# Kernel tuning notes

Measured on AMD Instinct MI355X. Metric: run time of the kernel, lower is better.

Reference implementation:

```python
import jax, jax.numpy as jnp
import numpy as np

EP = 1e-4
MAX_ITER = 100
NEG = -1e9
H = 8


def _layernorm(x, g, b, eps=1e-5):
    m = jnp.mean(x, axis=-1, keepdims=True)
    v = jnp.mean((x - m) ** 2, axis=-1, keepdims=True)
    return (x - m) * jax.lax.rsqrt(v + eps) * g + b


def _nonsat(x):
    # Fixed-point iteration y_{n+1} = (2 y^3/3 + x)/(y^2 + 1); torch detaches y each
    # step, so gradient only flows through x in the final update.
    xs = jax.lax.stop_gradient(x)

    def step(y):
        y2 = y * y
        return (2.0 * y * y2 / 3.0 + xs) / (y2 + 1.0)

    def cond(st):
        y, yn, i = st
        return jnp.logical_and(jnp.mean(jnp.abs(yn - y)) > EP, i <= MAX_ITER)

    def body(st):
        y, yn, i = st
        return (yn, step(yn), i + 1)

    y_prev, _, _ = jax.lax.while_loop(cond, body, (xs, step(xs), jnp.int32(0)))
    y2 = y_prev * y_prev
    return (2.0 * y_prev * y2 / 3.0 + x) / (y2 + 1.0)


def setup_inputs() -> dict:
    key = jax.random.key(0)
    ks = jax.random.split(key, 20)
    S, B, E = 256, 64, 512
    DH, SW, DSS, DFF, DEPTH = 512, 64, 128, 2048, 32
    sd = 0.02
    inp = {
        'x_in': jax.random.normal(ks[0], (S, B, E), jnp.float32),
        'stack_prev': jax.random.normal(ks[1], (B, S, DEPTH, SW), jnp.float32),
        'k_mask': jnp.zeros((B, S), jnp.bool_),
        'ln1_g': jnp.ones((E,), jnp.float32),
        'ln1_b': jnp.zeros((E,), jnp.float32),
        'in_proj_w': jax.random.normal(ks[2], (E, 3 * E), jnp.float32) * sd,
        'in_proj_b': jnp.zeros((3 * E,), jnp.float32),
        'out_w': jax.random.normal(ks[3], (E, E), jnp.float32) * sd,
        'out_b': jnp.zeros((E,), jnp.float32),
        'W_w': jax.random.normal(ks[4], (E, DH), jnp.float32) * sd,
        'W_b': jnp.zeros((DH,), jnp.float32),
        'P_w': jax.random.normal(ks[5], (SW, DH), jnp.float32) * sd,
        'P_b': jnp.zeros((DH,), jnp.float32),
        'V_w': jax.random.normal(ks[6], (E + DH, DSS), jnp.float32) * sd,
        'U_w': jax.random.normal(ks[7], (DSS, E), jnp.float32) * sd,
        'A_w': jax.random.normal(ks[8], (DH, 3), jnp.float32) * sd,
        'A_b': jnp.zeros((3,), jnp.float32),
        'D_w': jax.random.normal(ks[9], (DH, SW), jnp.float32) * sd,
        'D_b': jnp.zeros((SW,), jnp.float32),
        'ln2_g': jnp.ones((E,), jnp.float32),
        'ln2_b': jnp.zeros((E,), jnp.float32),
        'ff1_w': jax.random.normal(ks[10], (E, DFF), jnp.float32) * sd,
        'ff1_b': jnp.zeros((DFF,), jnp.float32),
        'ff2_w': jax.random.normal(ks[11], (DFF, E), jnp.float32) * sd,
        'ff2_b': jnp.zeros((E,), jnp.float32),
    }
    return inp


def reference(x_in, stack_prev, k_mask, ln1_g, ln1_b, in_proj_w, in_proj_b, out_w,
              out_b, W_w, W_b, P_w, P_b, V_w, U_w, A_w, A_b, D_w, D_b, ln2_g,
              ln2_b, ff1_w, ff1_b, ff2_w, ff2_b):
    S, B, E = x_in.shape
    hd = E // H
    scale = 1.0 / np.sqrt(hd)

    # --- sublayer 0: pre-norm causal self-attention ---
    xn = _layernorm(x_in, ln1_g, ln1_b)
    qkv = xn @ in_proj_w + in_proj_b            # (S,B,3E)
    q, k, v = jnp.split(qkv, 3, axis=-1)
    q = q.reshape(S, B, H, hd)
    k = k.reshape(S, B, H, hd)
    v = v.reshape(S, B, H, hd)
    scores = jnp.einsum('sbhd,tbhd->bhst', q, k) * scale
    causal = jnp.triu(jnp.full((S, S), NEG, x_in.dtype), k=1)
    scores = scores + causal
    scores = jnp.where(k_mask[:, None, None, :], NEG, scores)
    attn = jax.nn.softmax(scores, axis=-1)
    ao = jnp.einsum('bhst,tbhd->sbhd', attn, v).reshape(S, B, E)
    x = x_in + ao @ out_w + out_b

    # --- stack-augmented memory ---
    stack_x = stack_prev[:, :, 0, :]            # (B,S,SW) top of stack
    xb = jnp.transpose(x, (1, 0, 2))            # (B,S,E)
    hidden = _nonsat(xb @ W_w + W_b + stack_x @ P_w + P_b)  # (B,S,DH)
    vx = jnp.concatenate([x, jnp.transpose(hidden, (1, 0, 2))], axis=-1)
    y = jax.nn.softmax(vx @ V_w, axis=-1) @ U_w
    x = jnp.maximum(x, y)

    stack_inp = _nonsat(hidden @ D_w + D_b)[:, :, None, :]   # (B,S,1,SW)
    ctrl = jax.nn.softmax(hidden @ A_w + A_b, axis=-1)[..., None, None]  # (B,S,3,1,1)
    zeros = jnp.zeros_like(stack_prev[:, :, :1])
    stack_down = jnp.concatenate([stack_prev[:, :, 1:], zeros], axis=2)
    stack_up = jnp.concatenate([stack_inp, stack_prev[:, :, :-1]], axis=2)
    stack = ctrl[:, :, 2] * stack_prev + ctrl[:, :, 0] * stack_up + ctrl[:, :, 1] * stack_down

    # --- sublayer 1: pre-norm FFN ---
    xn2 = _layernorm(x, ln2_g, ln2_b)
    x = x + jax.nn.relu(xn2 @ ff1_w + ff1_b) @ ff2_w + ff2_b
    return (x, stack)
```

## Files before the change

kernel.cpp:

```cpp
#include <hip/hip_runtime.h>
#include <math.h>

#define S_DIM 256
#define B_DIM 64
#define E_DIM 512
#define H_NUM 8
#define HD 64
#define DH 512
#define SW 64
#define DSS 128
#define DFF 2048
#define DEPTH 32
#define M_ROWS 16384

typedef __attribute__((ext_vector_type(8))) short bf16x8;
typedef __attribute__((ext_vector_type(4))) float f32x4;

__device__ __forceinline__ ushort f2bf(float v){
    unsigned int u = __float_as_uint(v);
    u += 0x7fffu + ((u >> 16) & 1u);
    return (ushort)(u >> 16);
}
__device__ __forceinline__ float bf2f(ushort s){
    return __uint_as_float(((unsigned int)s) << 16);
}
__device__ __forceinline__ void splitbf(float v, ushort& h, ushort& l){
    h = f2bf(v);
    l = f2bf(v - bf2f(h));
}

__device__ __forceinline__ float nonsat_f(float x){
    float y = x;
#pragma unroll
    for (int i = 0; i < 10; i++){
        float y2 = y * y;
        y = (0.66666666f * y * y2 + x) / (y2 + 1.0f);
    }
    return y;
}

__global__ __launch_bounds__(256) void ln_split(const float* __restrict__ x,
                                                const float* __restrict__ g,
                                                const float* __restrict__ bta,
                                                ushort* __restrict__ oh,
                                                ushort* __restrict__ ol){
    __shared__ float red[4];
    int r = blockIdx.x;
    int t = threadIdx.x;
    const float* xr = x + (size_t)r * E_DIM;
    float v0 = xr[t], v1 = xr[t + 256];
    float s = v0 + v1;
#pragma unroll
    for (int off = 32; off > 0; off >>= 1) s += __shfl_xor(s, off, 64);
    if ((t & 63) == 0) red[t >> 6] = s;
    __syncthreads();
    float mean = (red[0] + red[1] + red[2] + red[3]) * (1.0f / 512.0f);
    __syncthreads();
    float d0 = v0 - mean, d1 = v1 - mean;
    float q = d0 * d0 + d1 * d1;
#pragma unroll
    for (int off = 32; off > 0; off >>= 1) q += __shfl_xor(q, off, 64);
    if ((t & 63) == 0) red[t >> 6] = q;
    __syncthreads();
    float var = (red[0] + red[1] + red[2] + red[3]) * (1.0f / 512.0f);
    float rs = rsqrtf(var + 1e-5f);
    size_t base = (size_t)r * E_DIM;
    float y0 = d0 * rs * g[t]       + bta[t];
    float y1 = d1 * rs * g[t + 256] + bta[t + 256];
    ushort h, l;
    splitbf(y0, h, l); oh[base + t] = h;       ol[base + t] = l;
    splitbf(y1, h, l); oh[base + t + 256] = h; ol[base + t + 256] = l;
}

__global__ __launch_bounds__(256) void wsplit_t(const float* __restrict__ W,
                                                ushort* __restrict__ th,
                                                ushort* __restrict__ tl,
                                                int K, int N){
    __shared__ float tile[32][33];
    int n0 = blockIdx.x << 5, k0 = blockIdx.y << 5;
    int tx = threadIdx.x & 31, ty = threadIdx.x >> 5;
#pragma unroll
    for (int i = 0; i < 32; i += 8)
        tile[ty + i][tx] = W[(size_t)(k0 + ty + i) * N + (n0 + tx)];
    __syncthreads();
#pragma unroll
    for (int i = 0; i < 32; i += 8){
        int n = ty + i;
        float v = tile[tx][n];
        ushort h, l; splitbf(v, h, l);
        th[(size_t)(n0 + n) * K + (k0 + tx)] = h;
        tl[(size_t)(n0 + n) * K + (k0 + tx)] = l;
    }
}

__global__ __launch_bounds__(256) void gemm_bf3(
    const ushort* __restrict__ Ah, const ushort* __restrict__ Al,
    const ushort* __restrict__ Bh, const ushort* __restrict__ Bl,
    const float* __restrict__ bias, const float* __restrict__ res,
    float* __restrict__ Cf, ushort* __restrict__ Ch, ushort* __restrict__ Cl,
    int M, int N, int K, int act, int resmode)
{
    __shared__ ushort lds[16384];
    const int tid = threadIdx.x;
    const int n0 = blockIdx.x << 7, m0 = blockIdx.y << 7;

    const int srow = tid >> 2, schunk = tid & 3;
    const int sOff = srow * 32 + (((srow + schunk) & 3) << 3);
    const ushort* gA0 = Ah + (size_t)(m0 + srow) * K + (schunk << 3);
    const ushort* gA1 = Al + (size_t)(m0 + srow) * K + (schunk << 3);
    const ushort* gB0 = Bh + (size_t)(n0 + srow) * K + (schunk << 3);
    const ushort* gB1 = Bl + (size_t)(n0 + srow) * K + (schunk << 3);
    const size_t rstep = (size_t)64 * K;

    const int lane = tid & 63;
    const int wv = tid >> 6;
    const int wm = (wv >> 1) << 6, wn = (wv & 1) << 6;
    const int r0 = lane & 15, gq = lane >> 4;
    const int gsub = (gq & 1) << 2;
    const int gc = gq >> 1;

    f32x4 acc[4][4];
    f32x4 zero = {0.f, 0.f, 0.f, 0.f};
#pragma unroll
    for (int i = 0; i < 4; i++)
#pragma unroll
        for (int j = 0; j < 4; j++) acc[i][j] = zero;

    uint4 v0,v1,v2,v3,v4,v5,v6,v7;
    v0 = *(const uint4*)(gA0);          v1 = *(const uint4*)(gA0 + rstep);
    v2 = *(const uint4*)(gA1);          v3 = *(const uint4*)(gA1 + rstep);
    v4 = *(const uint4*)(gB0);          v5 = *(const uint4*)(gB0 + rstep);
    v6 = *(const uint4*)(gB1);          v7 = *(const uint4*)(gB1 + rstep);

    for (int k0 = 0; k0 < K; k0 += 32){
        __syncthreads();
        *(uint4*)(&lds[sOff])               = v0;
        *(uint4*)(&lds[sOff + 2048])        = v1;
        *(uint4*)(&lds[4096 + sOff])        = v2;
        *(uint4*)(&lds[4096 + sOff + 2048]) = v3;
        *(uint4*)(&lds[8192 + sOff])        = v4;
        *(uint4*)(&lds[8192 + sOff + 2048]) = v5;
        *(uint4*)(&lds[12288 + sOff])        = v6;
        *(uint4*)(&lds[12288 + sOff + 2048]) = v7;
        __syncthreads();
        if (k0 + 32 < K){
            gA0 += 32; gA1 += 32; gB0 += 32; gB1 += 32;
            v0 = *(const uint4*)(gA0);  v1 = *(const uint4*)(gA0 + rstep);
            v2 = *(const uint4*)(gA1);  v3 = *(const uint4*)(gA1 + rstep);
            v4 = *(const uint4*)(gB0);  v5 = *(const uint4*)(gB0 + rstep);
            v6 = *(const uint4*)(gB1);  v7 = *(const uint4*)(gB1 + rstep);
        }
        bf16x8 fa[4], fal[4];
#pragma unroll
        for (int fr = 0; fr < 4; fr++){
            int R = wm + (fr << 4) + r0;
            int base = R * 32 + gsub;
            int c0 = ((gc + R) & 3) << 3;
            int c1 = ((gc + 2 + R) & 3) << 3;
            uint2 p0 = *(const uint2*)(&lds[base + c0]);
            uint2 p1 = *(const uint2*)(&lds[base + c1]);
            union { unsigned int u[4]; bf16x8 v; } t0;
            t0.u[0] = p0.x; t0.u[1] = p0.y; t0.u[2] = p1.x; t0.u[3] = p1.y;
            fa[fr] = t0.v;
            uint2 q0 = *(const uint2*)(&lds[4096 + base + c0]);
            uint2 q1 = *(const uint2*)(&lds[4096 + base + c1]);
            union { unsigned int u[4]; bf16x8 v; } t1;
            t1.u[0] = q0.x; t1.u[1] = q0.y; t1.u[2] = q1.x; t1.u[3] = q1.y;
            fal[fr] = t1.v;
        }
#pragma unroll
        for (int fc = 0; fc < 4; fc++){
            int R = wn + (fc << 4) + r0;
            int base = R * 32 + gsub;
            int c0 = ((gc + R) & 3) << 3;
            int c1 = ((gc + 2 + R) & 3) << 3;
            uint2 p0 = *(const uint2*)(&lds[8192 + base + c0]);
            uint2 p1 = *(const uint2*)(&lds[8192 + base + c1]);
            union { unsigned int u[4]; bf16x8 v; } t0;
            t0.u[0] = p0.x; t0.u[1] = p0.y; t0.u[2] = p1.x; t0.u[3] = p1.y;
            bf16x8 fbh = t0.v;
            uint2 q0 = *(const uint2*)(&lds[12288 + base + c0]);
            uint2 q1 = *(const uint2*)(&lds[12288 + base + c1]);
            union { unsigned int u[4]; bf16x8 v; } t1;
            t1.u[0] = q0.x; t1.u[1] = q0.y; t1.u[2] = q1.x; t1.u[3] = q1.y;
            bf16x8 fbl = t1.v;
#pragma unroll
            for (int fr = 0; fr < 4; fr++){
                acc[fr][fc] = __builtin_amdgcn_mfma_f32_16x16x32_bf16(fa[fr],  fbh, acc[fr][fc], 0, 0, 0);
                acc[fr][fc] = __builtin_amdgcn_mfma_f32_16x16x32_bf16(fa[fr],  fbl, acc[fr][fc], 0, 0, 0);
                acc[fr][fc] = __builtin_amdgcn_mfma_f32_16x16x32_bf16(fal[fr], fbh, acc[fr][fc], 0, 0, 0);
            }
        }
    }
#pragma unroll
    for (int fc = 0; fc < 4; fc++){
        int col = n0 + wn + (fc << 4) + r0;
        float bc = bias ? bias[col] : 0.f;
#pragma unroll
        for (int fr = 0; fr < 4; fr++){
#pragma unroll
            for (int e = 0; e < 4; e++){
                int row = m0 + wm + (fr << 4) + (gq << 2) + e;
                size_t idx = (size_t)row * N + col;
                float v = acc[fr][fc][e] + bc;
                if (resmode == 1) v += res[idx];
                else if (resmode == 2) v = fmaxf(v, res[idx]);
                if (act == 1) v = fmaxf(v, 0.f);
                if (Cf) Cf[idx] = v;
                if (Ch){ ushort hh, ll; splitbf(v, hh, ll); Ch[idx] = hh; Cl[idx] = ll; }
            }
        }
    }
}

__global__ __launch_bounds__(256) void gemm_k(const float* __restrict__ A,
                                              const float* __restrict__ W,
                                              const float* __restrict__ bias,
                                              const float* __restrict__ res,
                                              float* __restrict__ C,
                                              int M, int N, int K,
                                              int act, int resmode){
    __shared__ float As[32][68];
    __shared__ float Ws[32][68];
    int m0 = blockIdx.x << 6, n0 = blockIdx.y << 6;
    int tid = threadIdx.x;
    int tx = tid & 15, ty = tid >> 4;
    float acc[4][4] = {{0.f}};
    for (int k0 = 0; k0 < K; k0 += 32){
#pragma unroll
        for (int i = 0; i < 8; i++){
            int e = tid + (i << 8);
            int row = e >> 5, col = e & 31;
            As[col][row] = A[(size_t)(m0 + row) * K + (k0 + col)];
        }
#pragma unroll
        for (int i = 0; i < 8; i++){
            int e = tid + (i << 8);
            int kk = e >> 6, nn = e & 63;
            Ws[kk][nn] = W[(size_t)(k0 + kk) * N + (n0 + nn)];
        }
        __syncthreads();
#pragma unroll
        for (int kk = 0; kk < 32; kk++){
            float4 a = *(const float4*)(&As[kk][ty << 2]);
            float4 b = *(const float4*)(&Ws[kk][tx << 2]);
            float av[4] = {a.x, a.y, a.z, a.w};
            float bv[4] = {b.x, b.y, b.z, b.w};
#pragma unroll
            for (int i = 0; i < 4; i++)
#pragma unroll
                for (int j = 0; j < 4; j++) acc[i][j] = fmaf(av[i], bv[j], acc[i][j]);
        }
        __syncthreads();
    }
    int nbase = n0 + (tx << 2);
    float4 bv4 = make_float4(0.f, 0.f, 0.f, 0.f);
    if (bias) bv4 = *(const float4*)(bias + nbase);
#pragma unroll
    for (int i = 0; i < 4; i++){
        int mm = m0 + (ty << 2) + i;
        size_t idx = (size_t)mm * N + nbase;
        float v0 = acc[i][0] + bv4.x, v1 = acc[i][1] + bv4.y;
        float v2 = acc[i][2] + bv4.z, v3 = acc[i][3] + bv4.w;
        if (resmode == 1){
            float4 rv = *(const float4*)(res + idx);
            v0 += rv.x; v1 += rv.y; v2 += rv.z; v3 += rv.w;
        } else if (resmode == 2){
            float4 rv = *(const float4*)(res + idx);
            v0 = fmaxf(v0, rv.x); v1 = fmaxf(v1, rv.y);
            v2 = fmaxf(v2, rv.z); v3 = fmaxf(v3, rv.w);
        }
        if (act == 1){
            v0 = fmaxf(v0, 0.f); v1 = fmaxf(v1, 0.f);
            v2 = fmaxf(v2, 0.f); v3 = fmaxf(v3, 0.f);
        }
        *(float4*)(C + idx) = make_float4(v0, v1, v2, v3);
    }
}

__global__ __launch_bounds__(256) void gemm_hidden(const float* __restrict__ x1,
                                                   const float* __restrict__ stack_prev,
                                                   const float* __restrict__ Ww,
                                                   const float* __restrict__ Pw,
                                                   const float* __restrict__ Wb,
                                                   const float* __restrict__ Pb,
                                                   float* __restrict__ hidden){
    __shared__ float As[32][68];
    __shared__ float Ws[32][68];
    int m0 = blockIdx.x << 6, n0 = blockIdx.y << 6;
    int tid = threadIdx.x;
    int tx = tid & 15, ty = tid >> 4;
    float acc[4][4] = {{0.f}};
    for (int k0 = 0; k0 < 512; k0 += 32){
#pragma unroll
        for (int i = 0; i < 8; i++){
            int e = tid + (i << 8);
            int row = e >> 5, col = e & 31;
            int r = m0 + row;
            int xr = ((r & 255) << 6) | (r >> 8);
            As[col][row] = x1[(size_t)xr * 512 + (k0 + col)];
        }
#pragma unroll
        for (int i = 0; i < 8; i++){
            int e = tid + (i << 8);
            int kk = e >> 6, nn = e & 63;
            Ws[kk][nn] = Ww[(size_t)(k0 + kk) * 512 + (n0 + nn)];
        }
        __syncthreads();
#pragma unroll
        for (int kk = 0; kk < 32; kk++){
            float4 a = *(const float4*)(&As[kk][ty << 2]);
            float4 b = *(const float4*)(&Ws[kk][tx << 2]);
            float av[4] = {a.x, a.y, a.z, a.w};
            float bv[4] = {b.x, b.y, b.z, b.w};
#pragma unroll
            for (int i = 0; i < 4; i++)
#pragma unroll
                for (int j = 0; j < 4; j++) acc[i][j] = fmaf(av[i], bv[j], acc[i][j]);
        }
        __syncthreads();
    }
    for (int k0 = 0; k0 < 64; k0 += 32){
#pragma unroll
        for (int i = 0; i < 8; i++){
            int e = tid + (i << 8);
            int row = e >> 5, col = e & 31;
            As[col][row] = stack_prev[(size_t)(m0 + row) * 2048 + (k0 + col)];
        }
#pragma unroll
        for (int i = 0; i < 8; i++){
            int e = tid + (i << 8);
            int kk = e >> 6, nn = e & 63;
            Ws[kk][nn] = Pw[(size_t)(k0 + kk) * 512 + (n0 + nn)];
        }
        __syncthreads();
#pragma unroll
        for (int kk = 0; kk < 32; kk++){
            float4 a = *(const float4*)(&As[kk][ty << 2]);
            float4 b = *(const float4*)(&Ws[kk][tx << 2]);
            float av[4] = {a.x, a.y, a.z, a.w};
            float bv[4] = {b.x, b.y, b.z, b.w};
#pragma unroll
            for (int i = 0; i < 4; i++)
#pragma unroll
                for (int j = 0; j < 4; j++) acc[i][j] = fmaf(av[i], bv[j], acc[i][j]);
        }
        __syncthreads();
    }
    int nbase = n0 + (tx << 2);
#pragma unroll
    for (int i = 0; i < 4; i++){
        int mm = m0 + (ty << 2) + i;
        size_t idx = (size_t)mm * 512 + nbase;
        float4 o;
        o.x = nonsat_f(acc[i][0] + Wb[nbase]     + Pb[nbase]);
        o.y = nonsat_f(acc[i][1] + Wb[nbase + 1] + Pb[nbase + 1]);
        o.z = nonsat_f(acc[i][2] + Wb[nbase + 2] + Pb[nbase + 2]);
        o.w = nonsat_f(acc[i][3] + Wb[nbase + 3] + Pb[nbase + 3]);
        *(float4*)(hidden + idx) = o;
    }
}

__global__ __launch_bounds__(256) void gemm_vx(const float* __restrict__ x1,
                                               const float* __restrict__ hidden,
                                               const float* __restrict__ Vw,
                                               float* __restrict__ t){
    __shared__ float As[32][68];
    __shared__ float Ws[32][68];
    int m0 = blockIdx.x << 6, n0 = blockIdx.y << 6;
    int tid = threadIdx.x;
    int tx = tid & 15, ty = tid >> 4;
    float acc[4][4] = {{0.f}};
    for (int k0 = 0; k0 < 1024; k0 += 32){
        if (k0 < 512){
#pragma unroll
            for (int i = 0; i < 8; i++){
                int e = tid + (i << 8);
                int row = e >> 5, col = e & 31;
                As[col][row] = x1[(size_t)(m0 + row) * 512 + (k0 + col)];
            }
        } else {
#pragma unroll
            for (int i = 0; i < 8; i++){
                int e = tid + (i << 8);
                int row = e >> 5, col = e & 31;
                int r = m0 + row;
                int hr = ((r & 63) << 8) | (r >> 6);
                As[col][row] = hidden[(size_t)hr * 512 + (k0 - 512 + col)];
            }
        }
#pragma unroll
        for (int i = 0; i < 8; i++){
            int e = tid + (i << 8);
            int kk = e >> 6, nn = e & 63;
            Ws[kk][nn] = Vw[(size_t)(k0 + kk) * 128 + (n0 + nn)];
        }
        __syncthreads();
#pragma unroll
        for (int kk = 0; kk < 32; kk++){
            float4 a = *(const float4*)(&As[kk][ty << 2]);
            float4 b = *(const float4*)(&Ws[kk][tx << 2]);
            float av[4] = {a.x, a.y, a.z, a.w};
            float bv[4] = {b.x, b.y, b.z, b.w};
#pragma unroll
            for (int i = 0; i < 4; i++)
#pragma unroll
                for (int j = 0; j < 4; j++) acc[i][j] = fmaf(av[i], bv[j], acc[i][j]);
        }
        __syncthreads();
    }
    int nbase = n0 + (tx << 2);
#pragma unroll
    for (int i = 0; i < 4; i++){
        int mm = m0 + (ty << 2) + i;
        *(float4*)(t + (size_t)mm * 128 + nbase) =
            make_float4(acc[i][0], acc[i][1], acc[i][2], acc[i][3]);
    }
}

__global__ __launch_bounds__(128) void softmax128(float* __restrict__ t){
    __shared__ float red[2];
    int r = blockIdx.x, c = threadIdx.x;
    float v = t[(size_t)r * 128 + c];
    float m = v;
#pragma unroll
    for (int off = 32; off > 0; off >>= 1) m = fmaxf(m, __shfl_xor(m, off, 64));
    if ((c & 63) == 0) red[c >> 6] = m;
    __syncthreads();
    m = fmaxf(red[0], red[1]);
    __syncthreads();
    float e = expf(v - m);
    float s = e;
#pragma unroll
    for (int off = 32; off > 0; off >>= 1) s += __shfl_xor(s, off, 64);
    if ((c & 63) == 0) red[c >> 6] = s;
    __syncthreads();
    s = red[0] + red[1];
    t[(size_t)r * 128 + c] = e / s;
}

__global__ __launch_bounds__(256) void attn_kernel(const float* __restrict__ qkv,
                                                   ushort* __restrict__ aoh,
                                                   ushort* __restrict__ aol){
    __shared__ float Qs[64 * 68];
    __shared__ float KV[64 * 68];
    __shared__ float Ps[64 * 68];
    int bid = blockIdx.x;
    int ti = bid & 3, h = (bid >> 2) & 7, b = bid >> 5;
    int tid = threadIdx.x;
    int tx = tid & 15, ty = tid >> 4;
    const float scale = 0.125f;

    {
        const float* qbase = qkv + (size_t)b * 1536 + (h << 6);
#pragma unroll
        for (int i = 0; i < 4; i++){
            int f4 = tid + (i << 8);
            int r = f4 >> 4, c4 = f4 & 15;
            *(float4*)(&Qs[r * 68 + (c4 << 2)]) =
                *(const float4*)(qbase + (size_t)(((ti << 6) + r) << 6) * 1536 + (c4 << 2));
        }
    }
    float m_i[4], l_i[4], O[4][4];
#pragma unroll
    for (int i = 0; i < 4; i++){
        m_i[i] = -1e30f; l_i[i] = 0.f;
#pragma unroll
        for (int j = 0; j < 4; j++) O[i][j] = 0.f;
    }

    for (int tk = 0; tk <= ti; tk++){
        __syncthreads();
        {
            const float* kbase = qkv + (size_t)b * 1536 + 512 + (h << 6);
#pragma unroll
            for (int i = 0; i < 4; i++){
                int f4 = tid + (i << 8);
                int r = f4 >> 4, c4 = f4 & 15;
                *(float4*)(&KV[(r << 6) + (((c4 ^ (r >> 2)) & 15) << 2)]) =
                    *(const float4*)(kbase + (size_t)(((tk << 6) + r) << 6) * 1536 + (c4 << 2));
            }
        }
        __syncthreads();
        float sv[4][4] = {{0.f}};
#pragma unroll
        for (int d4 = 0; d4 < 16; d4++){
            float4 qa[4], kb[4];
#pragma unroll
            for (int i = 0; i < 4; i++)
                qa[i] = *(const float4*)(&Qs[((ty << 2) + i) * 68 + (d4 << 2)]);
#pragma unroll
            for (int j = 0; j < 4; j++)
                kb[j] = *(const float4*)(&KV[(((tx << 2) + j) << 6) + (((d4 ^ tx) & 15) << 2)]);
#pragma unroll
            for (int i = 0; i < 4; i++)
#pragma unroll
                for (int j = 0; j < 4; j++){
                    sv[i][j] = fmaf(qa[i].x, kb[j].x, sv[i][j]);
                    sv[i][j] = fmaf(qa[i].y, kb[j].y, sv[i][j]);
                    sv[i][j] = fmaf(qa[i].z, kb[j].z, sv[i][j]);
                    sv[i][j] = fmaf(qa[i].w, kb[j].w, sv[i][j]);
                }
        }
#pragma unroll
        for (int i = 0; i < 4; i++)
#pragma unroll
            for (int j = 0; j < 4; j++){
                float v = sv[i][j] * scale;
                if (tk == ti && ((tx << 2) + j) > ((ty << 2) + i)) v = -1e30f;
                sv[i][j] = v;
            }
        float alpha[4];
#pragma unroll
        for (int i = 0; i < 4; i++){
            float rm = fmaxf(fmaxf(sv[i][0], sv[i][1]), fmaxf(sv[i][2], sv[i][3]));
#pragma unroll
            for (int off = 8; off > 0; off >>= 1) rm = fmaxf(rm, __shfl_xor(rm, off, 64));
            float mn = fmaxf(m_i[i], rm);
            alpha[i] = __expf(m_i[i] - mn);
            float rs = 0.f;
#pragma unroll
            for (int j = 0; j < 4; j++){
                sv[i][j] = __expf(sv[i][j] - mn);
                rs += sv[i][j];
            }
#pragma unroll
            for (int off = 8; off > 0; off >>= 1) rs += __shfl_xor(rs, off, 64);
            l_i[i] = l_i[i] * alpha[i] + rs;
            m_i[i] = mn;
        }
#pragma unroll
        for (int i = 0; i < 4; i++)
            *(float4*)(&Ps[((ty << 2) + i) * 68 + (tx << 2)]) =
                make_float4(sv[i][0], sv[i][1], sv[i][2], sv[i][3]);
        __syncthreads();
        {
            const float* vbase = qkv + (size_t)b * 1536 + 1024 + (h << 6);
#pragma unroll
            for (int i = 0; i < 4; i++){
                int f4 = tid + (i << 8);
                int r = f4 >> 4, c4 = f4 & 15;
                *(float4*)(&KV[r * 68 + (c4 << 2)]) =
                    *(const float4*)(vbase + (size_t)(((tk << 6) + r) << 6) * 1536 + (c4 << 2));
            }
        }
        __syncthreads();
#pragma unroll
        for (int i = 0; i < 4; i++)
#pragma unroll
            for (int j = 0; j < 4; j++) O[i][j] *= alpha[i];
#pragma unroll
        for (int t4 = 0; t4 < 16; t4++){
            float4 pa[4], vb[4];
#pragma unroll
            for (int i = 0; i < 4; i++)
                pa[i] = *(const float4*)(&Ps[((ty << 2) + i) * 68 + (t4 << 2)]);
#pragma unroll
            for (int tt = 0; tt < 4; tt++)
                vb[tt] = *(const float4*)(&KV[((t4 << 2) + tt) * 68 + (tx << 2)]);
#pragma unroll
            for (int i = 0; i < 4; i++){
                float pav[4] = {pa[i].x, pa[i].y, pa[i].z, pa[i].w};
#pragma unroll
                for (int tt = 0; tt < 4; tt++){
                    O[i][0] = fmaf(pav[tt], vb[tt].x, O[i][0]);
                    O[i][1] = fmaf(pav[tt], vb[tt].y, O[i][1]);
                    O[i][2] = fmaf(pav[tt], vb[tt].z, O[i][2]);
                    O[i][3] = fmaf(pav[tt], vb[tt].w, O[i][3]);
                }
            }
        }
    }
#pragma unroll
    for (int i = 0; i < 4; i++){
        float inv = 1.0f / l_i[i];
        int sglob = (ti << 6) + (ty << 2) + i;
        size_t idx = (size_t)((sglob << 6) + b) * 512 + (h << 6) + (tx << 2);
        ushort4 hv, lv;
        float o0 = O[i][0] * inv, o1 = O[i][1] * inv, o2 = O[i][2] * inv, o3 = O[i][3] * inv;
        splitbf(o0, hv.x, lv.x);
        splitbf(o1, hv.y, lv.y);
        splitbf(o2, hv.z, lv.z);
        splitbf(o3, hv.w, lv.w);
        *(ushort4*)(aoh + idx) = hv;
        *(ushort4*)(aol + idx) = lv;
    }
}

__global__ __launch_bounds__(256) void stack_kernel(const float* __restrict__ hidden,
                                                    const float* __restrict__ stack_prev,
                                                    const float* __restrict__ Dw,
                                                    const float* __restrict__ Db,
                                                    const float* __restrict__ Aw,
                                                    const float* __restrict__ Ab,
                                                    float* __restrict__ stack_out){
    __shared__ float hs[512];
    __shared__ float sinp[64];
    __shared__ float aS[3];
    int r = blockIdx.x;
    int tid = threadIdx.x;
    hs[tid]       = hidden[(size_t)r * 512 + tid];
    hs[tid + 256] = hidden[(size_t)r * 512 + tid + 256];
    __syncthreads();
    if (tid < 64){
        float acc = Db[tid];
        for (int k = 0; k < 512; k++) acc = fmaf(hs[k], Dw[k * 64 + tid], acc);
        sinp[tid] = nonsat_f(acc);
    } else if (tid < 67){
        int c = tid - 64;
        float acc = Ab[c];
        for (int k = 0; k < 512; k++) acc = fmaf(hs[k], Aw[k * 3 + c], acc);
        aS[c] = acc;
    }
    __syncthreads();
    float a0 = aS[0], a1 = aS[1], a2 = aS[2];
    float mx = fmaxf(a0, fmaxf(a1, a2));
    float e0 = expf(a0 - mx), e1 = expf(a1 - mx), e2 = expf(a2 - mx);
    float inv = 1.f / (e0 + e1 + e2);
    float c0 = e0 * inv, c1 = e1 * inv, c2 = e2 * inv;
    const float* prow = stack_prev + (size_t)r * 2048;
    float* orow = stack_out + (size_t)r * 2048;
#pragma unroll
    for (int i = 0; i < 8; i++){
        int idx = tid + (i << 8);
        int dep = idx >> 6, j = idx & 63;
        float prev = prow[idx];
        float up   = dep ? prow[idx - 64] : sinp[j];
        float down = (dep < 31) ? prow[idx + 64] : 0.f;
        orow[idx] = c2 * prev + c0 * up + c1 * down;
    }
}

extern "C" void kernel_launch(void* const* d_in, const int* in_sizes, int n_in,
                              void* d_out, int out_size, void* d_ws, size_t ws_size,
                              hipStream_t stream){
    const float* x_in       = (const float*)d_in[0];
    const float* stack_prev = (const float*)d_in[1];
    const float* ln1_g = (const float*)d_in[3];
    const float* ln1_b = (const float*)d_in[4];
    const float* in_proj_w = (const float*)d_in[5];
    const float* in_proj_b = (const float*)d_in[6];
    const float* out_w = (const float*)d_in[7];
    const float* out_b = (const float*)d_in[8];
    const float* W_w = (const float*)d_in[9];
    const float* W_b = (const float*)d_in[10];
    const float* P_w = (const float*)d_in[11];
    const float* P_b = (const float*)d_in[12];
    const float* V_w = (const float*)d_in[13];
    const float* U_w = (const float*)d_in[14];
    const float* A_w = (const float*)d_in[15];
    const float* A_b = (const float*)d_in[16];
    const float* D_w = (const float*)d_in[17];
    const float* D_b = (const float*)d_in[18];
    const float* ln2_g = (const float*)d_in[19];
    const float* ln2_b = (const float*)d_in[20];
    const float* ff1_w = (const float*)d_in[21];
    const float* ff1_b = (const float*)d_in[22];
    const float* ff2_w = (const float*)d_in[23];
    const float* ff2_b = (const float*)d_in[24];

    float* dout_x     = (float*)d_out;
    float* dout_stack = dout_x + 8388608;
    float* qkv = dout_stack;
    float* x1  = dout_stack + 25165824;
    ushort* fmh = (ushort*)dout_stack;
    ushort* fml = fmh + 16777216;

    float* ws   = (float*)d_ws;
    float* bufA = ws;
    float* x2   = ws + 8388608;
    float* tbuf = ws + 16777216;
    ushort* xnh = (ushort*)(ws + 18874368);
    ushort* xnl = xnh + 8388608;
    ushort* wb0 = (ushort*)(ws + 27262976);
    ushort* ipTh = wb0;
    ushort* ipTl = ipTh + 786432;
    ushort* owTh = ipTl + 786432;
    ushort* owTl = owTh + 262144;
    ushort* f1Th = owTl + 262144;
    ushort* f1Tl = f1Th + 1048576;
    ushort* f2Th = f1Tl + 1048576;
    ushort* f2Tl = f2Th + 1048576;

    wsplit_t<<<dim3(48, 16), 256, 0, stream>>>(in_proj_w, ipTh, ipTl, 512, 1536);
    wsplit_t<<<dim3(16, 16), 256, 0, stream>>>(out_w, owTh, owTl, 512, 512);
    wsplit_t<<<dim3(64, 16), 256, 0, stream>>>(ff1_w, f1Th, f1Tl, 512, 2048);
    wsplit_t<<<dim3(16, 64), 256, 0, stream>>>(ff2_w, f2Th, f2Tl, 2048, 512);

    ln_split<<<16384, 256, 0, stream>>>(x_in, ln1_g, ln1_b, xnh, xnl);
    gemm_bf3<<<dim3(12, 128), 256, 0, stream>>>(xnh, xnl, ipTh, ipTl, in_proj_b, nullptr,
                                                qkv, nullptr, nullptr, 16384, 1536, 512, 0, 0);
    attn_kernel<<<2048, 256, 0, stream>>>(qkv, xnh, xnl);
    gemm_bf3<<<dim3(4, 128), 256, 0, stream>>>(xnh, xnl, owTh, owTl, out_b, x_in,
                                               x1, nullptr, nullptr, 16384, 512, 512, 0, 1);
    gemm_hidden<<<dim3(256, 8), 256, 0, stream>>>(x1, stack_prev, W_w, P_w, W_b, P_b, bufA);
    gemm_vx<<<dim3(256, 2), 256, 0, stream>>>(x1, bufA, V_w, tbuf);
    softmax128<<<16384, 128, 0, stream>>>(tbuf);
    gemm_k<<<dim3(256, 8), 256, 0, stream>>>(tbuf, U_w, nullptr, x1, x2,
                                             16384, 512, 128, 0, 2);
    ln_split<<<16384, 256, 0, stream>>>(x2, ln2_g, ln2_b, xnh, xnl);
    for (int c = 0; c < 2; c++){
        gemm_bf3<<<dim3(16, 64), 256, 0, stream>>>(xnh + c * 4194304, xnl + c * 4194304,
                                                   f1Th, f1Tl, ff1_b, nullptr,
                                                   nullptr, fmh, fml, 8192, 2048, 512, 1, 0);
        gemm_bf3<<<dim3(4, 64), 256, 0, stream>>>(fmh, fml, f2Th, f2Tl, ff2_b,
                                                  x2 + c * 4194304, dout_x + c * 4194304,
                                                  nullptr, nullptr, 8192, 512, 2048, 0, 1);
    }
    stack_kernel<<<16384, 256, 0, stream>>>(bufA, stack_prev, D_w, D_b, A_w, A_b, dout_stack);
}
```

Measured before the change: 1.612 ms.

## Move hidden GEMM to split-bf16 MFMA and batch stack head projections

Replaces the scalar fp32 hidden-state GEMM with a split-bf16 MFMA GEMM (three products per tile). It concatenates W_w and P_w into one pre-transposed K=576 weight and converts the stack-top fp32 values to hi/lo bf16 on the fly. The out-projection GEMM now also emits hi/lo bf16 copies of x1 to feed it. The per-row serial D/A matvecs inside the stack kernel are replaced by one batched GEMM into a padded 128-wide head buffer, so the stack kernel only applies nonsat, the 3-way softmax and the blend. The cost is extra workspace, extra prep kernels, and a three-pass bf16 approximation of fp32 accuracy for the hidden projection.

After: 1.512 ms. 6.2% less time.

```diff
diff --git a/kernel.cpp b/kernel.cpp
--- a/kernel.cpp
+++ b/kernel.cpp
@@ -75,7 +75,7 @@
 __global__ __launch_bounds__(256) void wsplit_t(const float* __restrict__ W,
                                                 ushort* __restrict__ th,
                                                 ushort* __restrict__ tl,
-                                                int K, int N){
+                                                int K, int N, int Ktot, int koff){
     __shared__ float tile[32][33];
     int n0 = blockIdx.x << 5, k0 = blockIdx.y << 5;
     int tx = threadIdx.x & 31, ty = threadIdx.x >> 5;
@@ -88,9 +88,35 @@
         int n = ty + i;
         float v = tile[tx][n];
         ushort h, l; splitbf(v, h, l);
-        th[(size_t)(n0 + n) * K + (k0 + tx)] = h;
-        tl[(size_t)(n0 + n) * K + (k0 + tx)] = l;
-    }
+        th[(size_t)(n0 + n) * Ktot + koff + k0 + tx] = h;
+        tl[(size_t)(n0 + n) * Ktot + koff + k0 + tx] = l;
+    }
+}
+
+__global__ __launch_bounds__(256) void build_dab(const float* __restrict__ Dw,
+                                                 const float* __restrict__ Db,
+                                                 const float* __restrict__ Aw,
+                                                 const float* __restrict__ Ab,
+                                                 const float* __restrict__ Wb,
+                                                 const float* __restrict__ Pb,
+                                                 float* __restrict__ DA,
+                                                 float* __restrict__ dabb,
+                                                 float* __restrict__ hbias){
+    int idx = blockIdx.x * 256 + threadIdx.x;
+    if (idx < 65536){
+        int k = idx >> 7, c = idx & 127;
+        float v = 0.f;
+        if (c < 64) v = Dw[k * 64 + c];
+        else if (c < 67) v = Aw[k * 3 + (c - 64)];
+        DA[idx] = v;
+    }
+    if (idx < 128){
+        float v = 0.f;
+        if (idx < 64) v = Db[idx];
+        else if (idx < 67) v = Ab[idx - 64];
+        dabb[idx] = v;
+    }
+    if (idx < 512) hbias[idx] = Wb[idx] + Pb[idx];
 }
 
 __global__ __launch_bounds__(256) void gemm_bf3(
@@ -206,8 +232,139 @@
                 if (resmode == 1) v += res[idx];
                 else if (resmode == 2) v = fmaxf(v, res[idx]);
                 if (act == 1) v = fmaxf(v, 0.f);
+                else if (act == 2) v = nonsat_f(v);
                 if (Cf) Cf[idx] = v;
                 if (Ch){ ushort hh, ll; splitbf(v, hh, ll); Ch[idx] = hh; Cl[idx] = ll; }
+            }
+        }
+    }
+}
+
+__global__ __launch_bounds__(256) void gemm_hidden_bf3(
+    const ushort* __restrict__ x1h, const ushort* __restrict__ x1l,
+    const float* __restrict__ stack_prev,
+    const ushort* __restrict__ Bh, const ushort* __restrict__ Bl,
+    const float* __restrict__ bias,
+    float* __restrict__ hidden)
+{
+    __shared__ ushort lds[16384];
+    const int tid = threadIdx.x;
+    const int n0 = blockIdx.x << 7, m0 = blockIdx.y << 7;
+    const int srow = tid >> 2, schunk = tid & 3;
+    const int sOff = srow * 32 + (((srow + schunk) & 3) << 3);
+    const int ra = m0 + srow, rb = m0 + 64 + srow;
+    const int xra = ((ra & 255) << 6) | (ra >> 8);
+    const int xrb = ((rb & 255) << 6) | (rb >> 8);
+    const ushort* gB0 = Bh + (size_t)(n0 + srow) * 576 + (schunk << 3);
+    const ushort* gB1 = Bl + (size_t)(n0 + srow) * 576 + (schunk << 3);
+    const size_t rstepB = (size_t)64 * 576;
+
+    const int lane = tid & 63;
+    const int wv = tid >> 6;
+    const int wm = (wv >> 1) << 6, wn = (wv & 1) << 6;
+    const int r0 = lane & 15, gq = lane >> 4;
+    const int gsub = (gq & 1) << 2;
+    const int gc = gq >> 1;
+
+    auto fetchA = [&](int k0, int row, int xr, uint4& vh, uint4& vl){
+        if (k0 < 512){
+            vh = *(const uint4*)(x1h + (size_t)xr * 512 + k0 + (schunk << 3));
+            vl = *(const uint4*)(x1l + (size_t)xr * 512 + k0 + (schunk << 3));
+        } else {
+            const float* sp = stack_prev + (size_t)row * 2048 + (k0 - 512) + (schunk << 3);
+            float f[8];
+            *(float4*)(f)     = *(const float4*)(sp);
+            *(float4*)(f + 4) = *(const float4*)(sp + 4);
+            union { ushort us[8]; uint4 u4; } th, tl;
+#pragma unroll
+            for (int j = 0; j < 8; j++) splitbf(f[j], th.us[j], tl.us[j]);
+            vh = th.u4; vl = tl.u4;
+        }
+    };
+
+    f32x4 acc[4][4];
+    f32x4 zero = {0.f, 0.f, 0.f, 0.f};
+#pragma unroll
+    for (int i = 0; i < 4; i++)
+#pragma unroll
+        for (int j = 0; j < 4; j++) acc[i][j] = zero;
+
+    uint4 v0,v1,v2,v3,v4,v5,v6,v7;
+    fetchA(0, ra, xra, v0, v2);
+    fetchA(0, rb, xrb, v1, v3);
+    v4 = *(const uint4*)(gB0); v5 = *(const uint4*)(gB0 + rstepB);
+    v6 = *(const uint4*)(gB1); v7 = *(const uint4*)(gB1 + rstepB);
+
+    for (int k0 = 0; k0 < 576; k0 += 32){
+        __syncthreads();
+        *(uint4*)(&lds[sOff])               = v0;
+        *(uint4*)(&lds[sOff + 2048])        = v1;
+        *(uint4*)(&lds[4096 + sOff])        = v2;
+        *(uint4*)(&lds[4096 + sOff + 2048]) = v3;
+        *(uint4*)(&lds[8192 + sOff])        = v4;
+        *(uint4*)(&lds[8192 + sOff + 2048]) = v5;
+        *(uint4*)(&lds[12288 + sOff])        = v6;
+        *(uint4*)(&lds[12288 + sOff + 2048]) = v7;
+        __syncthreads();
+        if (k0 + 32 < 576){
+            fetchA(k0 + 32, ra, xra, v0, v2);
+            fetchA(k0 + 32, rb, xrb, v1, v3);
+            gB0 += 32; gB1 += 32;
+            v4 = *(const uint4*)(gB0); v5 = *(const uint4*)(gB0 + rstepB);
+            v6 = *(const uint4*)(gB1); v7 = *(const uint4*)(gB1 + rstepB);
+        }
+        bf16x8 fa[4], fal[4];
+#pragma unroll
+        for (int fr = 0; fr < 4; fr++){
+            int R = wm + (fr << 4) + r0;
+            int base = R * 32 + gsub;
+            int c0 = ((gc + R) & 3) << 3;
+            int c1 = ((gc + 2 + R) & 3) << 3;
+            uint2 p0 = *(const uint2*)(&lds[base + c0]);
+            uint2 p1 = *(const uint2*)(&lds[base + c1]);
+            union { unsigned int u[4]; bf16x8 v; } t0;
+            t0.u[0] = p0.x; t0.u[1] = p0.y; t0.u[2] = p1.x; t0.u[3] = p1.y;
+            fa[fr] = t0.v;
+            uint2 q0 = *(const uint2*)(&lds[4096 + base + c0]);
+            uint2 q1 = *(const uint2*)(&lds[4096 + base + c1]);
+            union { unsigned int u[4]; bf16x8 v; } t1;
+            t1.u[0] = q0.x; t1.u[1] = q0.y; t1.u[2] = q1.x; t1.u[3] = q1.y;
+            fal[fr] = t1.v;
+        }
+#pragma unroll
+        for (int fc = 0; fc < 4; fc++){
+            int R = wn + (fc << 4) + r0;
+            int base = R * 32 + gsub;
+            int c0 = ((gc + R) & 3) << 3;
+            int c1 = ((gc + 2 + R) & 3) << 3;
+            uint2 p0 = *(const uint2*)(&lds[8192 + base + c0]);
+            uint2 p1 = *(const uint2*)(&lds[8192 + base + c1]);
+            union { unsigned int u[4]; bf16x8 v; } t0;
+            t0.u[0] = p0.x; t0.u[1] = p0.y; t0.u[2] = p1.x; t0.u[3] = p1.y;
+            bf16x8 fbh = t0.v;
+            uint2 q0 = *(const uint2*)(&lds[12288 + base + c0]);
+            uint2 q1 = *(const uint2*)(&lds[12288 + base + c1]);
+            union { unsigned int u[4]; bf16x8 v; } t1;
+            t1.u[0] = q0.x; t1.u[1] = q0.y; t1.u[2] = q1.x; t1.u[3] = q1.y;
+            bf16x8 fbl = t1.v;
+#pragma unroll
+            for (int fr = 0; fr < 4; fr++){
+                acc[fr][fc] = __builtin_amdgcn_mfma_f32_16x16x32_bf16(fa[fr],  fbh, acc[fr][fc], 0, 0, 0);
+                acc[fr][fc] = __builtin_amdgcn_mfma_f32_16x16x32_bf16(fa[fr],  fbl, acc[fr][fc], 0, 0, 0);
+                acc[fr][fc] = __builtin_amdgcn_mfma_f32_16x16x32_bf16(fal[fr], fbh, acc[fr][fc], 0, 0, 0);
+            }
+        }
+    }
+#pragma unroll
+    for (int fc = 0; fc < 4; fc++){
+        int col = n0 + wn + (fc << 4) + r0;
+        float bc = bias[col];
+#pragma unroll
+        for (int fr = 0; fr < 4; fr++){
+#pragma unroll
+            for (int e = 0; e < 4; e++){
+                int row = m0 + wm + (fr << 4) + (gq << 2) + e;
+                hidden[(size_t)row * 512 + col] = nonsat_f(acc[fr][fc][e] + bc);
             }
         }
     }
@@ -278,89 +435,6 @@
     }
 }
 
-__global__ __launch_bounds__(256) void gemm_hidden(const float* __restrict__ x1,
-                                                   const float* __restrict__ stack_prev,
-                                                   const float* __restrict__ Ww,
-                                                   const float* __restrict__ Pw,
-                                                   const float* __restrict__ Wb,
-                                                   const float* __restrict__ Pb,
-                                                   float* __restrict__ hidden){
-    __shared__ float As[32][68];
-    __shared__ float Ws[32][68];
-    int m0 = blockIdx.x << 6, n0 = blockIdx.y << 6;
-    int tid = threadIdx.x;
-    int tx = tid & 15, ty = tid >> 4;
-    float acc[4][4] = {{0.f}};
-    for (int k0 = 0; k0 < 512; k0 += 32){
-#pragma unroll
-        for (int i = 0; i < 8; i++){
-            int e = tid + (i << 8);
-            int row = e >> 5, col = e & 31;
-            int r = m0 + row;
-            int xr = ((r & 255) << 6) | (r >> 8);
-            As[col][row] = x1[(size_t)xr * 512 + (k0 + col)];
-        }
-#pragma unroll
-        for (int i = 0; i < 8; i++){
-            int e = tid + (i << 8);
-            int kk = e >> 6, nn = e & 63;
-            Ws[kk][nn] = Ww[(size_t)(k0 + kk) * 512 + (n0 + nn)];
-        }
-        __syncthreads();
-#pragma unroll
-        for (int kk = 0; kk < 32; kk++){
-            float4 a = *(const float4*)(&As[kk][ty << 2]);
-            float4 b = *(const float4*)(&Ws[kk][tx << 2]);
-            float av[4] = {a.x, a.y, a.z, a.w};
-            float bv[4] = {b.x, b.y, b.z, b.w};
-#pragma unroll
-            for (int i = 0; i < 4; i++)
-#pragma unroll
-                for (int j = 0; j < 4; j++) acc[i][j] = fmaf(av[i], bv[j], acc[i][j]);
-        }
-        __syncthreads();
-    }
-    for (int k0 = 0; k0 < 64; k0 += 32){
-#pragma unroll
-        for (int i = 0; i < 8; i++){
-            int e = tid + (i << 8);
-            int row = e >> 5, col = e & 31;
-            As[col][row] = stack_prev[(size_t)(m0 + row) * 2048 + (k0 + col)];
-        }
-#pragma unroll
-        for (int i = 0; i < 8; i++){
-            int e = tid + (i << 8);
-            int kk = e >> 6, nn = e & 63;
-            Ws[kk][nn] = Pw[(size_t)(k0 + kk) * 512 + (n0 + nn)];
-        }
-        __syncthreads();
-#pragma unroll
-        for (int kk = 0; kk < 32; kk++){
-            float4 a = *(const float4*)(&As[kk][ty << 2]);
-            float4 b = *(const float4*)(&Ws[kk][tx << 2]);
-            float av[4] = {a.x, a.y, a.z, a.w};
-            float bv[4] = {b.x, b.y, b.z, b.w};
-#pragma unroll
-            for (int i = 0; i < 4; i++)
-#pragma unroll
-                for (int j = 0; j < 4; j++) acc[i][j] = fmaf(av[i], bv[j], acc[i][j]);
-        }
-        __syncthreads();
-    }
-    int nbase = n0 + (tx << 2);
-#pragma unroll
-    for (int i = 0; i < 4; i++){
-        int mm = m0 + (ty << 2) + i;
-        size_t idx = (size_t)mm * 512 + nbase;
-        float4 o;
-        o.x = nonsat_f(acc[i][0] + Wb[nbase]     + Pb[nbase]);
-        o.y = nonsat_f(acc[i][1] + Wb[nbase + 1] + Pb[nbase + 1]);
-        o.z = nonsat_f(acc[i][2] + Wb[nbase + 2] + Pb[nbase + 2]);
-        o.w = nonsat_f(acc[i][3] + Wb[nbase + 3] + Pb[nbase + 3]);
-        *(float4*)(hidden + idx) = o;
-    }
-}
-
 __global__ __launch_bounds__(256) void gemm_vx(const float* __restrict__ x1,
                                                const float* __restrict__ hidden,
                                                const float* __restrict__ Vw,
@@ -587,37 +661,25 @@
     }
 }
 
-__global__ __launch_bounds__(256) void stack_kernel(const float* __restrict__ hidden,
+__global__ __launch_bounds__(256) void stack_update(const float* __restrict__ head,
                                                     const float* __restrict__ stack_prev,
-                                                    const float* __restrict__ Dw,
-                                                    const float* __restrict__ Db,
-                                                    const float* __restrict__ Aw,
-                                                    const float* __restrict__ Ab,
                                                     float* __restrict__ stack_out){
-    __shared__ float hs[512];
     __shared__ float sinp[64];
-    __shared__ float aS[3];
+    __shared__ float ctrl[3];
     int r = blockIdx.x;
     int tid = threadIdx.x;
-    hs[tid]       = hidden[(size_t)r * 512 + tid];
-    hs[tid + 256] = hidden[(size_t)r * 512 + tid + 256];
+    const float* hrow = head + (size_t)r * 128;
+    if (tid < 64){
+        sinp[tid] = nonsat_f(hrow[tid]);
+    } else if (tid == 64){
+        float a0 = hrow[64], a1 = hrow[65], a2 = hrow[66];
+        float mx = fmaxf(a0, fmaxf(a1, a2));
+        float e0 = expf(a0 - mx), e1 = expf(a1 - mx), e2 = expf(a2 - mx);
+        float inv = 1.f / (e0 + e1 + e2);
+        ctrl[0] = e0 * inv; ctrl[1] = e1 * inv; ctrl[2] = e2 * inv;
+    }
     __syncthreads();
-    if (tid < 64){
-        float acc = Db[tid];
-        for (int k = 0; k < 512; k++) acc = fmaf(hs[k], Dw[k * 64 + tid], acc);
-        sinp[tid] = nonsat_f(acc);
-    } else if (tid < 67){
-        int c = tid - 64;
-        float acc = Ab[c];
-        for (int k = 0; k < 512; k++) acc = fmaf(hs[k], Aw[k * 3 + c], acc);
-        aS[c] = acc;
-    }
-    __syncthreads();
-    float a0 = aS[0], a1 = aS[1], a2 = aS[2];
-    float mx = fmaxf(a0, fmaxf(a1, a2));
-    float e0 = expf(a0 - mx), e1 = expf(a1 - mx), e2 = expf(a2 - mx);
-    float inv = 1.f / (e0 + e1 + e2);
-    float c0 = e0 * inv, c1 = e1 * inv, c2 = e2 * inv;
+    float c0 = ctrl[0], c1 = ctrl[1], c2 = ctrl[2];
     const float* prow = stack_prev + (size_t)r * 2048;
     float* orow = stack_out + (size_t)r * 2048;
 #pragma unroll
@@ -663,7 +725,9 @@
     float* dout_stack = dout_x + 8388608;
     float* qkv = dout_stack;
     float* x1  = dout_stack + 25165824;
-    ushort* fmh = (ushort*)dout_stack;
+    ushort* x1h = (ushort*)dout_stack;
+    ushort* x1l = x1h + 8388608;
+    ushort* fmh = (ushort*)(dout_stack + 8388608);
     ushort* fml = fmh + 16777216;
 
     float* ws   = (float*)d_ws;
@@ -681,19 +745,31 @@
     ushort* f1Tl = f1Th + 1048576;
     ushort* f2Th = f1Tl + 1048576;
     ushort* f2Tl = f2Th + 1048576;
-
-    wsplit_t<<<dim3(48, 16), 256, 0, stream>>>(in_proj_w, ipTh, ipTl, 512, 1536);
-    wsplit_t<<<dim3(16, 16), 256, 0, stream>>>(out_w, owTh, owTl, 512, 512);
-    wsplit_t<<<dim3(64, 16), 256, 0, stream>>>(ff1_w, f1Th, f1Tl, 512, 2048);
-    wsplit_t<<<dim3(16, 64), 256, 0, stream>>>(ff2_w, f2Th, f2Tl, 2048, 512);
+    ushort* whT  = f2Tl + 1048576;
+    ushort* wlT  = whT + 294912;
+    float* headbuf = ws + 30703616;
+    float* DAw   = ws + 32800768;
+    float* dabb  = ws + 32866304;
+    float* hbias = ws + 32866432;
+
+    wsplit_t<<<dim3(48, 16), 256, 0, stream>>>(in_proj_w, ipTh, ipTl, 512, 1536, 512, 0);
+    wsplit_t<<<dim3(16, 16), 256, 0, stream>>>(out_w, owTh, owTl, 512, 512, 512, 0);
+    wsplit_t<<<dim3(64, 16), 256, 0, stream>>>(ff1_w, f1Th, f1Tl, 512, 2048, 512, 0);
+    wsplit_t<<<dim3(16, 64), 256, 0, stream>>>(ff2_w, f2Th, f2Tl, 2048, 512, 2048, 0);
+    wsplit_t<<<dim3(16, 16), 256, 0, stream>>>(W_w, whT, wlT, 512, 512, 576, 0);
+    wsplit_t<<<dim3(16, 2), 256, 0, stream>>>(P_w, whT, wlT, 64, 512, 576, 512);
+    build_dab<<<256, 256, 0, stream>>>(D_w, D_b, A_w, A_b, W_b, P_b, DAw, dabb, hbias);
 
     ln_split<<<16384, 256, 0, stream>>>(x_in, ln1_g, ln1_b, xnh, xnl);
     gemm_bf3<<<dim3(12, 128), 256, 0, stream>>>(xnh, xnl, ipTh, ipTl, in_proj_b, nullptr,
                                                 qkv, nullptr, nullptr, 16384, 1536, 512, 0, 0);
     attn_kernel<<<2048, 256, 0, stream>>>(qkv, xnh, xnl);
     gemm_bf3<<<dim3(4, 128), 256, 0, stream>>>(xnh, xnl, owTh, owTl, out_b, x_in,
-                                               x1, nullptr, nullptr, 16384, 512, 512, 0, 1);
-    gemm_hidden<<<dim3(256, 8), 256, 0, stream>>>(x1, stack_prev, W_w, P_w, W_b, P_b, bufA);
+                                               x1, x1h, x1l, 16384, 512, 512, 0, 1);
+    gemm_hidden_bf3<<<dim3(4, 128), 256, 0, stream>>>(x1h, x1l, stack_prev, whT, wlT,
+                                                      hbias, bufA);
+    gemm_k<<<dim3(256, 2), 256, 0, stream>>>(bufA, DAw, dabb, nullptr, headbuf,
+                                             16384, 128, 512, 0, 0);
     gemm_vx<<<dim3(256, 2), 256, 0, stream>>>(x1, bufA, V_w, tbuf);
     softmax128<<<16384, 128, 0, stream>>>(tbuf);
     gemm_k<<<dim3(256, 8), 256, 0, stream>>>(tbuf, U_w, nullptr, x1, x2,
@@ -707,5 +783,5 @@
                                                   x2 + c * 4194304, dout_x + c * 4194304,
                                                   nullptr, nullptr, 8192, 512, 2048, 0, 1);
     }
-    stack_kernel<<<16384, 256, 0, stream>>>(bufA, stack_prev, D_w, D_b, A_w, A_b, dout_stack);
-}
+    stack_update<<<16384, 256, 0, stream>>>(headbuf, stack_prev, dout_stack);
+}
```
